# Kernel tuning notes

Measured on AMD Instinct MI355X. Metric: run time of the kernel, lower is better.

The kernel has to match this reference:

```python
import jax, jax.numpy as jnp
import numpy as np

N_A, N_C, N_L = 50000, 10000, 10000
HID = 128


def _gatv2(x_src, x_dst, src, dst, ea, Wl, bl, Wr, br, We, att, bias, H):
    # GATv2Conv (PyG) bipartite, edge_dim=1, concat=False (mean over heads), eval mode (no dropout)
    C = bias.shape[0]
    n_dst = x_dst.shape[0]
    xl = (x_src @ Wl + bl).reshape(-1, H, C)      # [N_src, H, C]
    xr = (x_dst @ Wr + br).reshape(-1, H, C)      # [N_dst, H, C]
    e = jax.nn.leaky_relu(xl[src] + xr[dst] + (ea @ We).reshape(-1, H, C), 0.2)  # [E,H,C]
    logit = jnp.einsum('ehc,hc->eh', e, att)      # [E,H]
    m = jax.ops.segment_max(logit, dst, num_segments=n_dst)
    m = jax.lax.stop_gradient(jnp.where(jnp.isfinite(m), m, 0.0))
    ex = jnp.exp(logit - m[dst])
    denom = jax.ops.segment_sum(ex, dst, num_segments=n_dst)
    alpha = ex / (denom[dst] + 1e-16)             # segment softmax over incoming edges
    out = jax.ops.segment_sum(alpha[:, :, None] * xl[src], dst, num_segments=n_dst)
    return out.mean(axis=1) + bias                # concat=False -> head mean + bias


def setup_inputs() -> dict:
    key = jax.random.key(0)
    ks = iter(jax.random.split(key, 80))
    def rn(shape, s=1.0):
        return jax.random.normal(next(ks), shape, jnp.float32) * s
    inp = {}
    inp['x_asset'] = rn((N_A, 512))
    inp['x_creator'] = rn((N_C, 2))
    inp['x_licensee'] = rn((N_L, 1))
    # edges: (name, E, src_max, dst_max)
    edges = [('cb', 50000, N_A, N_C), ('lt', 100000, N_A, N_L), ('sim', 200000, N_A, N_A),
             ('fw', 100000, N_A, N_A), ('rcb', 50000, N_C, N_A), ('rlt', 100000, N_L, N_A)]
    for name, E, smax, dmax in edges:
        inp[f'{name}_src'] = jax.random.randint(next(ks), (E,), 0, smax, jnp.int32)
        inp[f'{name}_dst'] = jax.random.randint(next(ks), (E,), 0, dmax, jnp.int32)
        inp[f'ea_{name}'] = rn((E, 1))
    w = 0.05  # param scale
    inp['Wp_a'] = rn((512, HID), w); inp['bp_a'] = rn((HID,), w)
    inp['Wp_c'] = rn((2, HID), w);   inp['bp_c'] = rn((HID,), w)
    inp['Wp_l'] = rn((1, HID), w);   inp['bp_l'] = rn((HID,), w)
    # layer 1: heads=2, stacked over the 6 relations
    H1 = 2
    inp['Wl1'] = rn((6, HID, H1 * HID), w); inp['bl1'] = rn((6, H1 * HID), w)
    inp['Wr1'] = rn((6, HID, H1 * HID), w); inp['br1'] = rn((6, H1 * HID), w)
    inp['We1'] = rn((6, 1, H1 * HID), w)
    inp['att1'] = rn((6, H1, HID), w); inp['bias1'] = rn((6, HID), w)
    # layer 2: heads=1
    inp['Wl2'] = rn((6, HID, HID), w); inp['bl2'] = rn((6, HID), w)
    inp['Wr2'] = rn((6, HID, HID), w); inp['br2'] = rn((6, HID), w)
    inp['We2'] = rn((6, 1, HID), w)
    inp['att2'] = rn((6, 1, HID), w); inp['bias2'] = rn((6, HID), w)
    inp['Wc1'] = rn((HID, HID), w); inp['bc1'] = rn((HID,), w)
    inp['Wc2'] = rn((HID, 3), w);   inp['bc2'] = rn((3,), w)
    inp['query_asset_index'] = 123
    return inp


def reference(x_asset, x_creator, x_licensee, Wp_a, bp_a, Wp_c, bp_c, Wp_l, bp_l,
              Wl1, bl1, Wr1, br1, We1, att1, bias1,
              Wl2, bl2, Wr2, br2, We2, att2, bias2,
              Wc1, bc1, Wc2, bc2,
              ea_cb, ea_lt, ea_sim, ea_fw, ea_rcb, ea_rlt,
              cb_src, cb_dst, lt_src, lt_dst, sim_src, sim_dst,
              fw_src, fw_dst, rcb_src, rcb_dst, rlt_src, rlt_dst,
              query_asset_index):
    x = {'Asset': x_asset @ Wp_a + bp_a,
         'Creator': x_creator @ Wp_c + bp_c,
         'Licensee': x_licensee @ Wp_l + bp_l}
    rels = [('Asset', 'Creator', cb_src, cb_dst, ea_cb),
            ('Asset', 'Licensee', lt_src, lt_dst, ea_lt),
            ('Asset', 'Asset', sim_src, sim_dst, ea_sim),
            ('Asset', 'Asset', fw_src, fw_dst, ea_fw),
            ('Creator', 'Asset', rcb_src, rcb_dst, ea_rcb),
            ('Licensee', 'Asset', rlt_src, rlt_dst, ea_rlt)]

    def hetero_layer(x, Wl, bl, Wr, br, We, att, bias, H):
        out = {k: jnp.zeros((v.shape[0], HID), v.dtype) for k, v in x.items()}
        for i, (st, dt, s, d, ea) in enumerate(rels):  # HeteroConv aggr='sum'
            out[dt] = out[dt] + _gatv2(x[st], x[dt], s, d, ea,
                                       Wl[i], bl[i], Wr[i], br[i], We[i], att[i], bias[i], H)
        return out

    x = hetero_layer(x, Wl1, bl1, Wr1, br1, We1, att1, bias1, 2)
    x = {k: jax.nn.relu(v) for k, v in x.items()}  # eval: dropout is identity
    x = hetero_layer(x, Wl2, bl2, Wr2, br2, We2, att2, bias2, 1)
    x = {k: jax.nn.relu(v) for k, v in x.items()}
    a = x['Asset'][query_asset_index]
    return jax.nn.relu(a @ Wc1 + bc1) @ Wc2 + bc2
```

## Files before the change

### kernel.cpp

```cpp
#include <hip/hip_runtime.h>
#include <math.h>

#define FAMAX 64
#define FCMAX 32
#define FLMAX 32
#define N1MAX 512
#define N2MAX 128
#define PROJB 128
#define SCANB 512

struct Inputs {
  const float *x_asset, *x_creator, *x_licensee;
  const float *Wp_a,*bp_a,*Wp_c,*bp_c,*Wp_l,*bp_l;
  const float *Wl1,*bl1,*Wr1,*br1,*We1,*att1,*bias1;
  const float *Wl2,*bl2,*Wr2,*br2,*We2,*att2,*bias2;
  const float *Wc1,*bc1,*Wc2,*bc2;
};

struct Edges {
  const int *cb_s,*cb_d;  const float* ea_cb;  int Ecb;
  const int *lt_s,*lt_d;  const float* ea_lt;  int Elt;
  const int *sim_s,*sim_d;const float* ea_sim; int Esim;
  const int *fw_s,*fw_d;  const float* ea_fw;  int Efw;
  const int *rcb_s,*rcb_d;const float* ea_rcb; int Ercb;
  const int *rlt_s,*rlt_d;const float* ea_rlt; int Erlt;
};

struct WSP {
  int* cnt;
  int* nf;
  int* l2rel; int* l2src; float* l2ea; int* l2slot;
  int* l1rel; int* l1src; int* l1dslot; float* l1ea;
  float* xr1a;
  float* xr1c;
  float* xr1l;
  float* xl1e;
  float* logit1;
  float *x1a,*x1c,*x1l;
  float* xl2e;
  float* logit2;
};

__device__ __forceinline__ float leaky(float x){ return x > 0.f ? x : 0.2f*x; }

__device__ __forceinline__ int fsearch(const int* list, int n, int v){
  for (int k=0;k<n;k++) if (list[k]==v) return k;
  return -1;
}

__device__ __forceinline__ void proj256(int type, int node, const Inputs& in,
                                        float* h0, float* xs, float* part){
  int t = threadIdx.x;
  if (type == 0){
    xs[t]       = in.x_asset[(size_t)node*512 + t];
    xs[t + 256] = in.x_asset[(size_t)node*512 + t + 256];
    __syncthreads();
    int j = t & 127, g2 = t >> 7;
    float acc = 0.f;
    const float* W = in.Wp_a + (size_t)g2*256*128 + j;
    const float* xg = xs + g2*256;
    for (int k=0;k<256;k++) acc = fmaf(xg[k], W[(size_t)k*128], acc);
    part[t] = acc;
    __syncthreads();
    if (t < 128) h0[t] = in.bp_a[t] + part[t] + part[128 + t];
  } else if (type == 1){
    if (t < 128)
      h0[t] = in.bp_c[t] + in.x_creator[node*2]*in.Wp_c[t]
            + in.x_creator[node*2+1]*in.Wp_c[128+t];
  } else {
    if (t < 128)
      h0[t] = in.bp_l[t] + in.x_licensee[node]*in.Wp_l[t];
  }
  __syncthreads();
}

__device__ __forceinline__ void l2hit(int rel, int s, float e, WSP& w){
  int k = atomicAdd(&w.cnt[0], 1);
  if (k < N2MAX){ w.l2rel[k]=rel; w.l2src[k]=s; w.l2ea[k]=e; }
}

__device__ __forceinline__ void l2scan_rel(int rel, const int* sp, const int* dp,
                                           const float* ep, int E, int q,
                                           int gt, int gs, WSP& w){
  int nq = E >> 2;
  const int4* d4 = (const int4*)dp;
  for (int i = gt; i < nq; i += gs){
    int4 d = d4[i];
    int j = i << 2;
    if (d.x == q) l2hit(rel, sp[j],   ep[j],   w);
    if (d.y == q) l2hit(rel, sp[j+1], ep[j+1], w);
    if (d.z == q) l2hit(rel, sp[j+2], ep[j+2], w);
    if (d.w == q) l2hit(rel, sp[j+3], ep[j+3], w);
  }
  int base = nq << 2, tail = E - base;
  if (gt < tail){
    int j = base + gt;
    if (dp[j] == q) l2hit(rel, sp[j], ep[j], w);
  }
}

__device__ __forceinline__ void l1hit(int rel, int s, int slot, float e, WSP& w){
  int k = atomicAdd(&w.cnt[4], 1);
  if (k < N1MAX){ w.l1rel[k]=rel; w.l1src[k]=s; w.l1dslot[k]=slot; w.l1ea[k]=e; }
}

__device__ __forceinline__ void l1scan_rel(int rel, const int* sp, const int* dp,
                                           const float* ep, int E,
                                           const int* flist, int fn,
                                           int gt, int gs, WSP& w){
  int nq = E >> 2;
  const int4* d4 = (const int4*)dp;
  for (int i = gt; i < nq; i += gs){
    int4 d = d4[i];
    int j = i << 2;
    int s0 = fsearch(flist, fn, d.x); if (s0>=0) l1hit(rel, sp[j],   s0, ep[j],   w);
    int s1 = fsearch(flist, fn, d.y); if (s1>=0) l1hit(rel, sp[j+1], s1, ep[j+1], w);
    int s2 = fsearch(flist, fn, d.z); if (s2>=0) l1hit(rel, sp[j+2], s2, ep[j+2], w);
    int s3 = fsearch(flist, fn, d.w); if (s3>=0) l1hit(rel, sp[j+3], s3, ep[j+3], w);
  }
  int base = nq << 2, tail = E - base;
  if (gt < tail){
    int j = base + gt;
    int s0 = fsearch(flist, fn, dp[j]);
    if (s0>=0) l1hit(rel, sp[j], s0, ep[j], w);
  }
}

__global__ void __launch_bounds__(256) k1(Edges eg, const int* qptr, WSP w){
  int q = qptr[0];
  int gt = blockIdx.x*256 + threadIdx.x, gs = gridDim.x*256;
  l2scan_rel(2, eg.sim_s, eg.sim_d, eg.ea_sim, eg.Esim, q, gt, gs, w);
  l2scan_rel(3, eg.fw_s,  eg.fw_d,  eg.ea_fw,  eg.Efw,  q, gt, gs, w);
  l2scan_rel(4, eg.rcb_s, eg.rcb_d, eg.ea_rcb, eg.Ercb, q, gt, gs, w);
  l2scan_rel(5, eg.rlt_s, eg.rlt_d, eg.ea_rlt, eg.Erlt, q, gt, gs, w);
}

__global__ void __launch_bounds__(256) k2(Inputs in, Edges eg, WSP w, const int* qptr){
  __shared__ float xs[512], part[256], h0[128];
  __shared__ int s_fa[FAMAX], s_fc[FCMAX], s_fl[FLMAX];
  __shared__ int s_nf[3];
  __shared__ int s_l2rel[N2MAX], s_l2src[N2MAX], s_l2slot[N2MAX];
  int b = blockIdx.x, t = threadIdx.x;
  int q = qptr[0];
  int n2 = min(w.cnt[0], N2MAX);
  for (int i=t; i<n2; i+=256){ s_l2rel[i]=w.l2rel[i]; s_l2src[i]=w.l2src[i]; }
  __syncthreads();
  if (t==0){
    int nfa=0,nfc=0,nfl=0;
    s_fa[nfa++]=q;
    for (int i=0;i<n2;i++){
      int rel=s_l2rel[i], src=s_l2src[i], s=-1;
      if (rel<=3){ s=fsearch(s_fa,nfa,src); if (s<0 && nfa<FAMAX){ s=nfa; s_fa[nfa++]=src; } }
      else if (rel==4){ s=fsearch(s_fc,nfc,src); if (s<0 && nfc<FCMAX){ s=nfc; s_fc[nfc++]=src; } }
      else { s=fsearch(s_fl,nfl,src); if (s<0 && nfl<FLMAX){ s=nfl; s_fl[nfl++]=src; } }
      s_l2slot[i]=s;
    }
    s_nf[0]=nfa; s_nf[1]=nfc; s_nf[2]=nfl;
    if (b==0){
      w.nf[0]=nfa; w.nf[1]=nfc; w.nf[2]=nfl;
      for (int i=0;i<n2;i++) w.l2slot[i]=s_l2slot[i];
    }
  }
  __syncthreads();
  int nfa=s_nf[0], nfc=s_nf[1], nfl=s_nf[2];
  if (b < PROJB){
    int nf = nfa+nfc+nfl;
    if (b < nf){
      int type, slot, node;
      if (b<nfa){ type=0; slot=b; node=s_fa[slot]; }
      else if (b<nfa+nfc){ type=1; slot=b-nfa; node=s_fc[slot]; }
      else { type=2; slot=b-nfa-nfc; node=s_fl[slot]; }
      proj256(type, node, in, h0, xs, part);
      if (type==0){
        for (int rr=0; rr<4; rr++){
          int r = 2+rr;
          float acc = in.br1[r*256+t];
          const float* W = in.Wr1 + (size_t)r*128*256 + t;
          for (int c=0;c<128;c++) acc = fmaf(h0[c], W[(size_t)c*256], acc);
          w.xr1a[((size_t)slot*4+rr)*256 + t] = acc;
        }
      } else if (type==1){
        float acc = in.br1[t];
        const float* W = in.Wr1 + t;
        for (int c=0;c<128;c++) acc = fmaf(h0[c], W[(size_t)c*256], acc);
        w.xr1c[(size_t)slot*256+t] = acc;
      } else {
        float acc = in.br1[256+t];
        const float* W = in.Wr1 + (size_t)128*256 + t;
        for (int c=0;c<128;c++) acc = fmaf(h0[c], W[(size_t)c*256], acc);
        w.xr1l[(size_t)slot*256+t] = acc;
      }
    }
    return;
  }
  int gt = (b-PROJB)*256 + t, gs = SCANB*256;
  l1scan_rel(0, eg.cb_s,  eg.cb_d,  eg.ea_cb,  eg.Ecb,  s_fc, nfc, gt, gs, w);
  l1scan_rel(1, eg.lt_s,  eg.lt_d,  eg.ea_lt,  eg.Elt,  s_fl, nfl, gt, gs, w);
  l1scan_rel(2, eg.sim_s, eg.sim_d, eg.ea_sim, eg.Esim, s_fa, nfa, gt, gs, w);
  l1scan_rel(3, eg.fw_s,  eg.fw_d,  eg.ea_fw,  eg.Efw,  s_fa, nfa, gt, gs, w);
  l1scan_rel(4, eg.rcb_s, eg.rcb_d, eg.ea_rcb, eg.Ercb, s_fa, nfa, gt, gs, w);
  l1scan_rel(5, eg.rlt_s, eg.rlt_d, eg.ea_rlt, eg.Erlt, s_fa, nfa, gt, gs, w);
}

__global__ void __launch_bounds__(256) k3(Inputs in, WSP w){
  __shared__ float xs[512], part[256], h0[128];
  __shared__ float pr[4];
  int t = threadIdx.x;
  int n1 = min(w.cnt[4], N1MAX);
  for (int e = blockIdx.x; e < n1; e += gridDim.x){
    int rel = w.l1rel[e], src = w.l1src[e], dslot = w.l1dslot[e];
    float ea = w.l1ea[e];
    int stype = (rel<=3)?0:(rel==4?1:2);
    proj256(stype, src, in, h0, xs, part);
    float xl1 = in.bl1[rel*256+t];
    {
      const float* W = in.Wl1 + (size_t)rel*128*256 + t;
      for (int c=0;c<128;c++) xl1 = fmaf(h0[c], W[(size_t)c*256], xl1);
    }
    w.xl1e[(size_t)e*256+t] = xl1;
    float xr1 = (rel==0) ? w.xr1c[(size_t)dslot*256+t]
              : (rel==1) ? w.xr1l[(size_t)dslot*256+t]
              : w.xr1a[((size_t)dslot*4 + (rel-2))*256 + t];
    float ev = leaky(xl1 + xr1 + ea*in.We1[rel*256+t]);
    float rd = ev * in.att1[(rel*2 + (t>>7))*128 + (t&127)];
    for (int off=32; off; off>>=1) rd += __shfl_down(rd, off);
    if ((t&63)==0) pr[t>>6] = rd;
    __syncthreads();
    if (t==0){ w.logit1[2*e]=pr[0]+pr[1]; w.logit1[2*e+1]=pr[2]+pr[3]; }
    __syncthreads();
  }
}

__global__ void __launch_bounds__(128) k4a(Inputs in, WSP w){
  __shared__ int   s_key[N1MAX];
  __shared__ float s_lg0[N1MAX], s_lg1[N1MAX];
  __shared__ int   s_list[4][N1MAX];
  __shared__ int   s_c[4];
  int b = blockIdx.x, t = threadIdx.x;
  int nfa = w.nf[0], nfc = w.nf[1], nfl = w.nf[2];
  int nf = nfa+nfc+nfl;
  if (b >= nf) return;
  int type, slot;
  if (b<nfa){ type=0; slot=b; }
  else if (b<nfa+nfc){ type=1; slot=b-nfa; }
  else { type=2; slot=b-nfa-nfc; }
  int n1 = min(w.cnt[4], N1MAX);
  if (t<4) s_c[t]=0;
  __syncthreads();
  for (int i=t;i<n1;i+=128){
    s_key[i] = (w.l1rel[i]<<6) | w.l1dslot[i];
    s_lg0[i] = w.logit1[2*i];
    s_lg1[i] = w.logit1[2*i+1];
  }
  __syncthreads();
  int r0,r1;
  if (type==0){ r0=2;r1=5; } else if (type==1){ r0=0;r1=0; } else { r0=1;r1=1; }
  for (int i=t;i<n1;i+=128){
    int key=s_key[i], rel=key>>6, sl=key&63;
    if (sl==slot && rel>=r0 && rel<=r1){
      int li = rel - r0;
      int pos = atomicAdd(&s_c[li],1);
      s_list[li][pos]=i;
    }
  }
  __syncthreads();
  float out=0.f;
  for (int r=r0;r<=r1;r++){
    out += in.bias1[r*128+t];
    int c = s_c[r-r0];
    if (c==0) continue;
    const int* lst = s_list[r-r0];
    float m0=-INFINITY,m1=-INFINITY;
    for (int o=0;o<c;o++){
      int i=lst[o];
      m0=fmaxf(m0,s_lg0[i]); m1=fmaxf(m1,s_lg1[i]);
    }
    float d0=0.f,d1=0.f,a0=0.f,a1=0.f;
    for (int o=0;o<c;o++){
      int i=lst[o];
      float e0=expf(s_lg0[i]-m0), e1=expf(s_lg1[i]-m1);
      d0+=e0; d1+=e1;
      a0=fmaf(e0, w.xl1e[(size_t)i*256+t],     a0);
      a1=fmaf(e1, w.xl1e[(size_t)i*256+128+t], a1);
    }
    out += 0.5f*(a0/(d0+1e-16f)+a1/(d1+1e-16f));
  }
  float v=fmaxf(out,0.f);
  if (type==0) w.x1a[(size_t)slot*128+t]=v;
  else if (type==1) w.x1c[(size_t)slot*128+t]=v;
  else w.x1l[(size_t)slot*128+t]=v;
}

__global__ void __launch_bounds__(128) k4b(Inputs in, WSP w){
  __shared__ float xq[128], xsrc[128];
  __shared__ float pr[2];
  int e = blockIdx.x, t = threadIdx.x;
  int n2 = min(w.cnt[0], N2MAX);
  if (e >= n2) return;
  int rel = w.l2rel[e], slot = w.l2slot[e];
  float ea = w.l2ea[e];
  if (slot < 0){
    w.xl2e[(size_t)e*128+t]=0.f;
    if (t==0) w.logit2[e]=-INFINITY;
    return;
  }
  const float* xb = (rel<=3)? w.x1a : (rel==4? w.x1c : w.x1l);
  xq[t]   = w.x1a[t];
  xsrc[t] = xb[(size_t)slot*128+t];
  __syncthreads();
  float xr2 = in.br2[rel*128+t];
  {
    const float* W = in.Wr2 + (size_t)rel*128*128 + t;
    for (int c=0;c<128;c++) xr2 = fmaf(xq[c], W[(size_t)c*128], xr2);
  }
  float xl2 = in.bl2[rel*128+t];
  {
    const float* W = in.Wl2 + (size_t)rel*128*128 + t;
    for (int c=0;c<128;c++) xl2 = fmaf(xsrc[c], W[(size_t)c*128], xl2);
  }
  w.xl2e[(size_t)e*128+t]=xl2;
  float ev = leaky(xl2 + xr2 + ea*in.We2[rel*128+t]);
  float rd = ev * in.att2[rel*128+t];
  for (int off=32;off;off>>=1) rd += __shfl_down(rd,off);
  if ((t&63)==0) pr[t>>6]=rd;
  __syncthreads();
  if (t==0) w.logit2[e]=pr[0]+pr[1];
}

__global__ void __launch_bounds__(128) k4c(Inputs in, WSP w, float* outp){
  __shared__ float x2[128], hid[128];
  __shared__ int   s_rel[N2MAX];
  __shared__ float s_lg[N2MAX];
  int t = threadIdx.x;
  int n2 = min(w.cnt[0], N2MAX);
  for (int i=t;i<n2;i+=128){ s_rel[i]=w.l2rel[i]; s_lg[i]=w.logit2[i]; }
  __syncthreads();
  float o=0.f;
  for (int r=2;r<=5;r++){
    o += in.bias2[r*128+t];
    float m=-INFINITY;
    for (int i=0;i<n2;i++) if (s_rel[i]==r) m=fmaxf(m,s_lg[i]);
    if (m==-INFINITY) continue;
    float d=0.f, acc=0.f;
    for (int i=0;i<n2;i++) if (s_rel[i]==r){
      float e=expf(s_lg[i]-m);
      d+=e;
      acc=fmaf(e, w.xl2e[(size_t)i*128+t], acc);
    }
    o += acc/(d+1e-16f);
  }
  x2[t]=fmaxf(o,0.f);
  __syncthreads();
  float a=in.bc1[t];
  for (int c=0;c<128;c++) a=fmaf(x2[c], in.Wc1[c*128+t], a);
  hid[t]=fmaxf(a,0.f);
  __syncthreads();
  if (t<3){
    float r=in.bc2[t];
    for (int c=0;c<128;c++) r=fmaf(hid[c], in.Wc2[c*3+t], r);
    outp[t]=r;
  }
}

extern "C" void kernel_launch(void* const* d_in, const int* in_sizes, int n_in,
                              void* d_out, int out_size, void* d_ws, size_t ws_size,
                              hipStream_t stream){
  Inputs in;
  in.x_asset   = (const float*)d_in[0];
  in.x_creator = (const float*)d_in[1];
  in.x_licensee= (const float*)d_in[2];
  Edges eg;
  eg.cb_s =(const int*)d_in[3];  eg.cb_d =(const int*)d_in[4];  eg.ea_cb =(const float*)d_in[5];  eg.Ecb = in_sizes[3];
  eg.lt_s =(const int*)d_in[6];  eg.lt_d =(const int*)d_in[7];  eg.ea_lt =(const float*)d_in[8];  eg.Elt = in_sizes[6];
  eg.sim_s=(const int*)d_in[9];  eg.sim_d=(const int*)d_in[10]; eg.ea_sim=(const float*)d_in[11]; eg.Esim= in_sizes[9];
  eg.fw_s =(const int*)d_in[12]; eg.fw_d =(const int*)d_in[13]; eg.ea_fw =(const float*)d_in[14]; eg.Efw = in_sizes[12];
  eg.rcb_s=(const int*)d_in[15]; eg.rcb_d=(const int*)d_in[16]; eg.ea_rcb=(const float*)d_in[17]; eg.Ercb= in_sizes[15];
  eg.rlt_s=(const int*)d_in[18]; eg.rlt_d=(const int*)d_in[19]; eg.ea_rlt=(const float*)d_in[20]; eg.Erlt= in_sizes[18];
  in.Wp_a=(const float*)d_in[21]; in.bp_a=(const float*)d_in[22];
  in.Wp_c=(const float*)d_in[23]; in.bp_c=(const float*)d_in[24];
  in.Wp_l=(const float*)d_in[25]; in.bp_l=(const float*)d_in[26];
  in.Wl1=(const float*)d_in[27]; in.bl1=(const float*)d_in[28];
  in.Wr1=(const float*)d_in[29]; in.br1=(const float*)d_in[30];
  in.We1=(const float*)d_in[31]; in.att1=(const float*)d_in[32]; in.bias1=(const float*)d_in[33];
  in.Wl2=(const float*)d_in[34]; in.bl2=(const float*)d_in[35];
  in.Wr2=(const float*)d_in[36]; in.br2=(const float*)d_in[37];
  in.We2=(const float*)d_in[38]; in.att2=(const float*)d_in[39]; in.bias2=(const float*)d_in[40];
  in.Wc1=(const float*)d_in[41]; in.bc1=(const float*)d_in[42];
  in.Wc2=(const float*)d_in[43]; in.bc2=(const float*)d_in[44];
  const int* qptr = (const int*)d_in[45];
  float* outp = (float*)d_out;

  char* p = (char*)d_ws;
  auto carve = [&](size_t n)->char*{ char* r = p; p += ((n + 255) & ~(size_t)255); return r; };
  WSP w;
  w.cnt  = (int*)carve(16*4);
  w.nf   = (int*)carve(3*4);
  w.l2rel=(int*)carve(N2MAX*4); w.l2src=(int*)carve(N2MAX*4);
  w.l2ea=(float*)carve(N2MAX*4); w.l2slot=(int*)carve(N2MAX*4);
  w.l1rel=(int*)carve(N1MAX*4); w.l1src=(int*)carve(N1MAX*4);
  w.l1dslot=(int*)carve(N1MAX*4); w.l1ea=(float*)carve(N1MAX*4);
  w.xr1a=(float*)carve((size_t)FAMAX*4*256*4);
  w.xr1c=(float*)carve((size_t)FCMAX*256*4);
  w.xr1l=(float*)carve((size_t)FLMAX*256*4);
  w.xl1e=(float*)carve((size_t)N1MAX*256*4);
  w.logit1=(float*)carve((size_t)N1MAX*2*4);
  w.x1a=(float*)carve((size_t)FAMAX*128*4);
  w.x1c=(float*)carve((size_t)FCMAX*128*4);
  w.x1l=(float*)carve((size_t)FLMAX*128*4);
  w.xl2e=(float*)carve((size_t)N2MAX*128*4);
  w.logit2=(float*)carve(N2MAX*4);

  hipMemsetAsync(w.cnt, 0, 64, stream);

  int quad2 = (eg.Esim + eg.Efw + eg.Ercb + eg.Erlt)/4 + 1;
  int b1 = (quad2 + 255)/256; if (b1 > 1024) b1 = 1024;
  k1<<<b1, 256, 0, stream>>>(eg, qptr, w);
  k2<<<PROJB + SCANB, 256, 0, stream>>>(in, eg, w, qptr);
  k3<<<256, 256, 0, stream>>>(in, w);
  k4a<<<FAMAX + FCMAX + FLMAX, 128, 0, stream>>>(in, w);
  k4b<<<N2MAX, 128, 0, stream>>>(in, w);
  k4c<<<1, 128, 0, stream>>>(in, w, outp);
}
```

Baseline: 294.8 us.

## Prefetch weights into L2 during edge scan and widen tail kernels to 256 threads

Adds extra blocks to the first edge-scan kernel that stream all weight matrices through a dummy reduction, warming the L2/MALL cache for later kernels. The layer-1 aggregation, layer-2 edge projection and classifier kernels move to 256 threads, splitting heads or the reduction dimension across two halves with a shared-memory combine. Logit loads are vectorised as float2. The prefetch adds extra memory traffic and blocks that compete with the scan, and the split reductions add barriers.

```diff
diff --git a/kernel.cpp b/kernel.cpp
--- a/kernel.cpp
+++ b/kernel.cpp
@@ -8,6 +8,7 @@
 #define N2MAX 128
 #define PROJB 128
 #define SCANB 512
+#define PFB   96
 
 struct Inputs {
   const float *x_asset, *x_creator, *x_licensee;
@@ -48,6 +49,14 @@
   return -1;
 }
 
+__device__ __forceinline__ float pf4(const float* p, int n, int gt, int gs){
+  float s = 0.f;
+  const float4* p4 = (const float4*)p;
+  int n4 = n >> 2;
+  for (int i = gt; i < n4; i += gs){ float4 v = p4[i]; s += v.x+v.y+v.z+v.w; }
+  return s;
+}
+
 __device__ __forceinline__ void proj256(int type, int node, const Inputs& in,
                                         float* h0, float* xs, float* part){
   int t = threadIdx.x;
@@ -126,9 +135,34 @@
   }
 }
 
-__global__ void __launch_bounds__(256) k1(Edges eg, const int* qptr, WSP w){
+__global__ void __launch_bounds__(256) k1(Edges eg, Inputs in, const int* qptr,
+                                          WSP w, int scanB){
+  if ((int)blockIdx.x >= scanB){
+    int gt = (blockIdx.x - scanB)*256 + threadIdx.x, gs = PFB*256;
+    float s = 0.f;
+    s += pf4(in.Wp_a, 512*128, gt, gs);
+    s += pf4(in.Wr1, 6*128*256, gt, gs);
+    s += pf4(in.Wl1, 6*128*256, gt, gs);
+    s += pf4(in.Wr2, 6*128*128, gt, gs);
+    s += pf4(in.Wl2, 6*128*128, gt, gs);
+    s += pf4(in.Wc1, 128*128, gt, gs);
+    s += pf4(in.We1, 6*256, gt, gs);
+    s += pf4(in.att1, 6*256, gt, gs);
+    s += pf4(in.bl1, 6*256, gt, gs);
+    s += pf4(in.br1, 6*256, gt, gs);
+    s += pf4(in.bias1, 6*128, gt, gs);
+    s += pf4(in.We2, 6*128, gt, gs);
+    s += pf4(in.att2, 6*128, gt, gs);
+    s += pf4(in.bias2, 6*128, gt, gs);
+    s += pf4(in.bl2, 6*128, gt, gs);
+    s += pf4(in.br2, 6*128, gt, gs);
+    s += pf4(in.Wc2, 128*3, gt, gs);
+    s += pf4(in.bc1, 128, gt, gs);
+    asm volatile("" :: "v"(s));
+    return;
+  }
   int q = qptr[0];
-  int gt = blockIdx.x*256 + threadIdx.x, gs = gridDim.x*256;
+  int gt = blockIdx.x*256 + threadIdx.x, gs = scanB*256;
   l2scan_rel(2, eg.sim_s, eg.sim_d, eg.ea_sim, eg.Esim, q, gt, gs, w);
   l2scan_rel(3, eg.fw_s,  eg.fw_d,  eg.ea_fw,  eg.Efw,  q, gt, gs, w);
   l2scan_rel(4, eg.rcb_s, eg.rcb_d, eg.ea_rcb, eg.Ercb, q, gt, gs, w);
@@ -231,11 +265,12 @@
   }
 }
 
-__global__ void __launch_bounds__(128) k4a(Inputs in, WSP w){
+__global__ void __launch_bounds__(256) k4a(Inputs in, WSP w){
   __shared__ int   s_key[N1MAX];
   __shared__ float s_lg0[N1MAX], s_lg1[N1MAX];
   __shared__ int   s_list[4][N1MAX];
   __shared__ int   s_c[4];
+  __shared__ float sA[256];
   int b = blockIdx.x, t = threadIdx.x;
   int nfa = w.nf[0], nfc = w.nf[1], nfl = w.nf[2];
   int nf = nfa+nfc+nfl;
@@ -247,15 +282,15 @@
   int n1 = min(w.cnt[4], N1MAX);
   if (t<4) s_c[t]=0;
   __syncthreads();
-  for (int i=t;i<n1;i+=128){
+  for (int i=t;i<n1;i+=256){
     s_key[i] = (w.l1rel[i]<<6) | w.l1dslot[i];
-    s_lg0[i] = w.logit1[2*i];
-    s_lg1[i] = w.logit1[2*i+1];
+    float2 L = ((const float2*)w.logit1)[i];
+    s_lg0[i] = L.x; s_lg1[i] = L.y;
   }
   __syncthreads();
   int r0,r1;
   if (type==0){ r0=2;r1=5; } else if (type==1){ r0=0;r1=0; } else { r0=1;r1=1; }
-  for (int i=t;i<n1;i+=128){
+  for (int i=t;i<n1;i+=256){
     int key=s_key[i], rel=key>>6, sl=key&63;
     if (sl==slot && rel>=r0 && rel<=r1){
       int li = rel - r0;
@@ -264,35 +299,40 @@
     }
   }
   __syncthreads();
-  float out=0.f;
+  int j = t&127, h = t>>7;
+  const float* lg = h ? s_lg1 : s_lg0;
+  float out = 0.f;
   for (int r=r0;r<=r1;r++){
-    out += in.bias1[r*128+t];
-    int c = s_c[r-r0];
-    if (c==0) continue;
-    const int* lst = s_list[r-r0];
-    float m0=-INFINITY,m1=-INFINITY;
-    for (int o=0;o<c;o++){
-      int i=lst[o];
-      m0=fmaxf(m0,s_lg0[i]); m1=fmaxf(m1,s_lg1[i]);
-    }
-    float d0=0.f,d1=0.f,a0=0.f,a1=0.f;
-    for (int o=0;o<c;o++){
-      int i=lst[o];
-      float e0=expf(s_lg0[i]-m0), e1=expf(s_lg1[i]-m1);
-      d0+=e0; d1+=e1;
-      a0=fmaf(e0, w.xl1e[(size_t)i*256+t],     a0);
-      a1=fmaf(e1, w.xl1e[(size_t)i*256+128+t], a1);
-    }
-    out += 0.5f*(a0/(d0+1e-16f)+a1/(d1+1e-16f));
-  }
-  float v=fmaxf(out,0.f);
-  if (type==0) w.x1a[(size_t)slot*128+t]=v;
-  else if (type==1) w.x1c[(size_t)slot*128+t]=v;
-  else w.x1l[(size_t)slot*128+t]=v;
-}
-
-__global__ void __launch_bounds__(128) k4b(Inputs in, WSP w){
-  __shared__ float xq[128], xsrc[128];
+    int li = r-r0, c = s_c[li];
+    float av = 0.f;
+    if (c>0){
+      const int* lst = s_list[li];
+      float m=-INFINITY;
+      for (int o=0;o<c;o++) m = fmaxf(m, lg[lst[o]]);
+      float d=0.f, a=0.f;
+      for (int o=0;o<c;o++){
+        int i = lst[o];
+        float e = expf(lg[i]-m);
+        d += e;
+        a = fmaf(e, w.xl1e[(size_t)i*256 + h*128 + j], a);
+      }
+      av = a/(d+1e-16f);
+    }
+    sA[t] = av;
+    __syncthreads();
+    if (t<128) out += in.bias1[r*128+j] + 0.5f*(sA[j]+sA[j+128]);
+    __syncthreads();
+  }
+  if (t<128){
+    float v = fmaxf(out, 0.f);
+    if (type==0) w.x1a[(size_t)slot*128+j]=v;
+    else if (type==1) w.x1c[(size_t)slot*128+j]=v;
+    else w.x1l[(size_t)slot*128+j]=v;
+  }
+}
+
+__global__ void __launch_bounds__(256) k4b(Inputs in, WSP w){
+  __shared__ float xq[128], xsrc[128], px[256], pl[256];
   __shared__ float pr[2];
   int e = blockIdx.x, t = threadIdx.x;
   int n2 = min(w.cnt[0], N2MAX);
@@ -300,60 +340,71 @@
   int rel = w.l2rel[e], slot = w.l2slot[e];
   float ea = w.l2ea[e];
   if (slot < 0){
-    w.xl2e[(size_t)e*128+t]=0.f;
+    if (t<128) w.xl2e[(size_t)e*128+t]=0.f;
     if (t==0) w.logit2[e]=-INFINITY;
     return;
   }
   const float* xb = (rel<=3)? w.x1a : (rel==4? w.x1c : w.x1l);
-  xq[t]   = w.x1a[t];
-  xsrc[t] = xb[(size_t)slot*128+t];
-  __syncthreads();
-  float xr2 = in.br2[rel*128+t];
+  if (t<128){ xq[t] = w.x1a[t]; xsrc[t] = xb[(size_t)slot*128+t]; }
+  __syncthreads();
+  int j = t&127, g = t>>7;
+  float axr=0.f, axl=0.f;
   {
-    const float* W = in.Wr2 + (size_t)rel*128*128 + t;
-    for (int c=0;c<128;c++) xr2 = fmaf(xq[c], W[(size_t)c*128], xr2);
-  }
-  float xl2 = in.bl2[rel*128+t];
-  {
-    const float* W = in.Wl2 + (size_t)rel*128*128 + t;
-    for (int c=0;c<128;c++) xl2 = fmaf(xsrc[c], W[(size_t)c*128], xl2);
-  }
-  w.xl2e[(size_t)e*128+t]=xl2;
-  float ev = leaky(xl2 + xr2 + ea*in.We2[rel*128+t]);
-  float rd = ev * in.att2[rel*128+t];
+    const float* Wr = in.Wr2 + (size_t)rel*128*128 + j;
+    const float* Wl = in.Wl2 + (size_t)rel*128*128 + j;
+    for (int c=g*64; c<g*64+64; c++){
+      axr = fmaf(xq[c],   Wr[(size_t)c*128], axr);
+      axl = fmaf(xsrc[c], Wl[(size_t)c*128], axl);
+    }
+  }
+  px[t]=axr; pl[t]=axl;
+  __syncthreads();
+  float rd = 0.f;
+  if (t<128){
+    float xr2 = in.br2[rel*128+j] + px[j] + px[j+128];
+    float xl2 = in.bl2[rel*128+j] + pl[j] + pl[j+128];
+    w.xl2e[(size_t)e*128+j] = xl2;
+    float ev = leaky(xl2 + xr2 + ea*in.We2[rel*128+j]);
+    rd = ev * in.att2[rel*128+j];
+  }
   for (int off=32;off;off>>=1) rd += __shfl_down(rd,off);
-  if ((t&63)==0) pr[t>>6]=rd;
-  __syncthreads();
-  if (t==0) w.logit2[e]=pr[0]+pr[1];
-}
-
-__global__ void __launch_bounds__(128) k4c(Inputs in, WSP w, float* outp){
-  __shared__ float x2[128], hid[128];
+  if ((t&63)==0 && t<128) pr[t>>6]=rd;
+  __syncthreads();
+  if (t==0) w.logit2[e] = pr[0]+pr[1];
+}
+
+__global__ void __launch_bounds__(256) k4c(Inputs in, WSP w, float* outp){
+  __shared__ float x2[128], hid[128], part[256];
   __shared__ int   s_rel[N2MAX];
   __shared__ float s_lg[N2MAX];
   int t = threadIdx.x;
   int n2 = min(w.cnt[0], N2MAX);
-  for (int i=t;i<n2;i+=128){ s_rel[i]=w.l2rel[i]; s_lg[i]=w.logit2[i]; }
-  __syncthreads();
-  float o=0.f;
-  for (int r=2;r<=5;r++){
-    o += in.bias2[r*128+t];
-    float m=-INFINITY;
-    for (int i=0;i<n2;i++) if (s_rel[i]==r) m=fmaxf(m,s_lg[i]);
-    if (m==-INFINITY) continue;
-    float d=0.f, acc=0.f;
-    for (int i=0;i<n2;i++) if (s_rel[i]==r){
-      float e=expf(s_lg[i]-m);
-      d+=e;
-      acc=fmaf(e, w.xl2e[(size_t)i*128+t], acc);
-    }
-    o += acc/(d+1e-16f);
-  }
-  x2[t]=fmaxf(o,0.f);
-  __syncthreads();
-  float a=in.bc1[t];
-  for (int c=0;c<128;c++) a=fmaf(x2[c], in.Wc1[c*128+t], a);
-  hid[t]=fmaxf(a,0.f);
+  for (int i=t;i<n2;i+=256){ s_rel[i]=w.l2rel[i]; s_lg[i]=w.logit2[i]; }
+  __syncthreads();
+  if (t<128){
+    float o=0.f;
+    for (int r=2;r<=5;r++){
+      o += in.bias2[r*128+t];
+      float m=-INFINITY;
+      for (int i=0;i<n2;i++) if (s_rel[i]==r) m=fmaxf(m,s_lg[i]);
+      if (m==-INFINITY) continue;
+      float d=0.f, acc=0.f;
+      for (int i=0;i<n2;i++) if (s_rel[i]==r){
+        float e=expf(s_lg[i]-m);
+        d+=e;
+        acc=fmaf(e, w.xl2e[(size_t)i*128+t], acc);
+      }
+      o += acc/(d+1e-16f);
+    }
+    x2[t]=fmaxf(o,0.f);
+  }
+  __syncthreads();
+  int j = t&127, g = t>>7;
+  float a=0.f;
+  for (int c=g*64;c<g*64+64;c++) a=fmaf(x2[c], in.Wc1[(size_t)c*128+j], a);
+  part[t]=a;
+  __syncthreads();
+  if (t<128) hid[t]=fmaxf(in.bc1[t]+part[t]+part[t+128], 0.f);
   __syncthreads();
   if (t<3){
     float r=in.bc2[t];
@@ -414,10 +465,10 @@
 
   int quad2 = (eg.Esim + eg.Efw + eg.Ercb + eg.Erlt)/4 + 1;
   int b1 = (quad2 + 255)/256; if (b1 > 1024) b1 = 1024;
-  k1<<<b1, 256, 0, stream>>>(eg, qptr, w);
+  k1<<<b1 + PFB, 256, 0, stream>>>(eg, in, qptr, w, b1);
   k2<<<PROJB + SCANB, 256, 0, stream>>>(in, eg, w, qptr);
   k3<<<256, 256, 0, stream>>>(in, w);
-  k4a<<<FAMAX + FCMAX + FLMAX, 128, 0, stream>>>(in, w);
-  k4b<<<N2MAX, 128, 0, stream>>>(in, w);
-  k4c<<<1, 128, 0, stream>>>(in, w, outp);
-}
+  k4a<<<FAMAX + FCMAX + FLMAX, 256, 0, stream>>>(in, w);
+  k4b<<<N2MAX, 256, 0, stream>>>(in, w);
+  k4c<<<1, 256, 0, stream>>>(in, w, outp);
+}
```

Measured after the change: 288.1 us. -2.3%, faster.
